# Kernel optimization log

Measured on AMD Instinct MI355X. Metric: run time of the kernel, lower is better.

## Reference

```python
import jax, jax.numpy as jnp
import numpy as np
from jax import lax

B, T, C = 32, 4096, 64
K, D, H, OUT = 256, 64, 512, 6

def _conv1d(x, w, b, stride):
    # x: [B, Cin, L], w: [Cout, Cin, k]
    y = lax.conv_general_dilated(x, w, (stride,), 'SAME',
                                 dimension_numbers=('NCH', 'OIH', 'NCH'))
    return y + b[None, :, None]

def _lstm_layer(x, wih, whh, b):
    # x: [B, T, in]; wih: [4H, in]; whh: [4H, H]
    Bb = x.shape[0]
    Hh = whh.shape[1]
    xg = jnp.einsum('bti,gi->btg', x, wih) + b          # [B, T, 4H] precomputed input gates
    def step(carry, g_t):
        h, c = carry
        gates = g_t + h @ whh.T
        i, f, g, o = jnp.split(gates, 4, axis=-1)        # torch gate order i,f,g,o
        i = jax.nn.sigmoid(i); f = jax.nn.sigmoid(f)
        g = jnp.tanh(g);       o = jax.nn.sigmoid(o)
        c = f * c + i * g
        h = o * jnp.tanh(c)
        return (h, c), h
    init = (jnp.zeros((Bb, Hh), x.dtype), jnp.zeros((Bb, Hh), x.dtype))
    _, hs = lax.scan(step, init, jnp.swapaxes(xg, 0, 1))
    return jnp.swapaxes(hs, 0, 1)                        # [B, T, H]

def setup_inputs() -> dict:
    key = jax.random.key(0)
    ks = jax.random.split(key, 12)
    s = 0.02
    return {
        'x':       jax.random.normal(ks[0], (B, T, C), jnp.float32),
        'conv_w1': jax.random.normal(ks[1], (64, 1, 4), jnp.float32) * s,
        'conv_b1': jnp.zeros((64,), jnp.float32),
        'conv_w2': jax.random.normal(ks[2], (64, 64, 4), jnp.float32) * s,
        'conv_b2': jnp.zeros((64,), jnp.float32),
        'conv_w3': jax.random.normal(ks[3], (64, 64, 3), jnp.float32) * s,
        'conv_b3': jnp.zeros((64,), jnp.float32),
        'codebook': jax.random.normal(ks[4], (K, D), jnp.float32),
        'wih0': jax.random.normal(ks[5], (4 * H, D), jnp.float32) * s,
        'whh0': jax.random.normal(ks[6], (4 * H, H), jnp.float32) * s,
        'bl0':  jnp.zeros((4 * H,), jnp.float32),
        'wih1': jax.random.normal(ks[7], (4 * H, H), jnp.float32) * s,
        'whh1': jax.random.normal(ks[8], (4 * H, H), jnp.float32) * s,
        'bl1':  jnp.zeros((4 * H,), jnp.float32),
        'w_out': jax.random.normal(ks[9], (OUT, H), jnp.float32) * s,
        'b_out': jnp.zeros((OUT,), jnp.float32),
    }

def reference(x, conv_w1, conv_b1, conv_w2, conv_b2, conv_w3, conv_b3,
              codebook, wih0, whh0, bl0, wih1, whh1, bl1, w_out, b_out):
    # ---- tokenizer (batched; replaces the per-sample python loop) ----
    sig = x.mean(axis=2)[:, None, :]                     # [B, 1, T] channel-mean 1D signal
    h1 = jax.nn.relu(_conv1d(sig, conv_w1, conv_b1, 2))   # [B, 64, T/2]
    h2 = jax.nn.relu(_conv1d(h1, conv_w2, conv_b2, 2))    # [B, 64, T/4]
    ze = _conv1d(h2, conv_w3, conv_b3, 1)                 # [B, D, T'] latents
    ze = jnp.swapaxes(ze, 1, 2)                           # [B, T', D]
    # nearest-code lookup: ||z - e||^2 argmin
    d = (jnp.sum(ze * ze, -1, keepdims=True)
         - 2.0 * ze @ codebook.T
         + jnp.sum(codebook * codebook, -1)[None, None, :])
    idx = jnp.argmin(d, axis=-1)                          # [B, T'] token indices
    # ---- codebook embedding gather ----
    z = codebook[idx]                                     # [B, T', D]
    # ---- 2-layer LSTM + per-step linear head ----
    h = _lstm_layer(z, wih0, whh0, bl0)
    h = _lstm_layer(h, wih1, whh1, bl1)
    preds = jnp.einsum('bth,oh->bto', h, w_out) + b_out   # [B, T', OUT]
    return preds
```

## Files before the change

kernel.cpp:

```cpp
#include <hip/hip_runtime.h>

constexpr int nB = 32, nT = 4096, nK = 256, nTP = 1024;

__device__ __forceinline__ float sigmoidf_(float x) { return 1.f / (1.f + expf(-x)); }

typedef unsigned int u32x4 __attribute__((ext_vector_type(4)));

__device__ __forceinline__ void store_u32_wt(unsigned* p, unsigned v) {
  asm volatile("global_store_dword %0, %1, off sc0 sc1" :: "v"(p), "v"(v) : "memory");
}
__device__ __forceinline__ void store_f32_wt(float* p, float v) {
  asm volatile("global_store_dword %0, %1, off sc0 sc1" :: "v"(p), "v"(v) : "memory");
}

__device__ __forceinline__ float dpp_xor1(float x) {
  return __int_as_float(__builtin_amdgcn_update_dpp(0, __float_as_int(x), 0xB1, 0xF, 0xF, true));
}
__device__ __forceinline__ float dpp_xor2(float x) {
  return __int_as_float(__builtin_amdgcn_update_dpp(0, __float_as_int(x), 0x4E, 0xF, 0xF, true));
}
__device__ __forceinline__ float dpp_xor8(float x) {
  return __int_as_float(__builtin_amdgcn_update_dpp(0, __float_as_int(x), 0x128, 0xF, 0xF, true));
}
__device__ __forceinline__ float swz_xor4(float x) {
  return __int_as_float(__builtin_amdgcn_ds_swizzle(__float_as_int(x), 0x101F));
}
__device__ __forceinline__ float swz_xor16(float x) {
  return __int_as_float(__builtin_amdgcn_ds_swizzle(__float_as_int(x), 0x401F));
}


__global__ __launch_bounds__(256) void k_mean(const float* __restrict__ x, float* __restrict__ sig) {
  int row = blockIdx.x * 4 + (threadIdx.x >> 6);
  int lane = threadIdx.x & 63;
  float v = x[(size_t)row * 64 + lane];
  #pragma unroll
  for (int off = 32; off > 0; off >>= 1) v += __shfl_down(v, off, 64);
  if (lane == 0) sig[row] = v * (1.0f / 64.0f);
}

__global__ __launch_bounds__(256) void k_conv1(const float* __restrict__ sig,
    const float* __restrict__ w1, const float* __restrict__ b1, float* __restrict__ h1) {
  int idx = blockIdx.x * 256 + threadIdx.x;
  int o = idx & 2047;
  int co = (idx >> 11) & 63;
  int b = idx >> 17;
  const float* s = sig + (size_t)b * nT;
  float acc = b1[co];
  int base = 2 * o - 1;
  #pragma unroll
  for (int j = 0; j < 4; j++) {
    int p = base + j;
    float sv = (p >= 0 && p < nT) ? s[p] : 0.f;
    acc = fmaf(w1[co * 4 + j], sv, acc);
  }
  h1[idx] = fmaxf(acc, 0.f);
}

__global__ __launch_bounds__(256) void k_conv2(const float* __restrict__ h1,
    const float* __restrict__ w2, const float* __restrict__ b2, float* __restrict__ h2) {
  int blk = blockIdx.x;
  int otile = blk & 3, co = (blk >> 2) & 63, b = blk >> 8;
  int o = otile * 256 + threadIdx.x;
  __shared__ float w[256];
  w[threadIdx.x] = w2[co * 256 + threadIdx.x];
  __syncthreads();
  const float* hin = h1 + (size_t)b * 64 * 2048;
  float acc = b2[co];
  int base = 2 * o - 1;
  for (int ci = 0; ci < 64; ci++) {
    const float* r = hin + ci * 2048;
    const float* wc = w + ci * 4;
    #pragma unroll
    for (int j = 0; j < 4; j++) {
      int p = base + j;
      float v = (p >= 0 && p < 2048) ? r[p] : 0.f;
      acc = fmaf(wc[j], v, acc);
    }
  }
  h2[((size_t)b * 64 + co) * 1024 + o] = fmaxf(acc, 0.f);
}

__global__ __launch_bounds__(256) void k_conv3(const float* __restrict__ h2,
    const float* __restrict__ w3, const float* __restrict__ b3, float* __restrict__ ze) {
  int blk = blockIdx.x;
  int otile = blk & 3, co = (blk >> 2) & 63, b = blk >> 8;
  int o = otile * 256 + threadIdx.x;
  __shared__ float w[192];
  if (threadIdx.x < 192) w[threadIdx.x] = w3[co * 192 + threadIdx.x];
  __syncthreads();
  const float* hin = h2 + (size_t)b * 64 * 1024;
  float acc = b3[co];
  for (int ci = 0; ci < 64; ci++) {
    const float* r = hin + ci * 1024;
    const float* wc = w + ci * 3;
    #pragma unroll
    for (int j = 0; j < 3; j++) {
      int p = o - 1 + j;
      float v = (p >= 0 && p < 1024) ? r[p] : 0.f;
      acc = fmaf(wc[j], v, acc);
    }
  }
  ze[((size_t)b * 64 + co) * 1024 + o] = acc;
}

__global__ __launch_bounds__(256) void k_cbnorm(const float* __restrict__ cb, float* __restrict__ cbn) {
  int k = threadIdx.x;
  const float4* c4 = (const float4*)(cb + (size_t)k * 64);
  float acc = 0.f;
  #pragma unroll
  for (int q = 0; q < 16; q++) {
    float4 e = c4[q];
    acc = fmaf(e.x, e.x, fmaf(e.y, e.y, fmaf(e.z, e.z, fmaf(e.w, e.w, acc))));
  }
  cbn[k] = acc;
}

__global__ __launch_bounds__(256) void k_vq(const float* __restrict__ ze,
    const float* __restrict__ cb, const float* __restrict__ cbn, float* __restrict__ zq) {
  __shared__ float scb[nK * 64];
  for (int i = threadIdx.x; i < nK * 64; i += 256) scb[i] = cb[i];
  __syncthreads();
  int g = blockIdx.x * 256 + threadIdx.x;
  int b = g >> 10, o = g & 1023;
  const float* zb = ze + (size_t)b * 64 * 1024 + o;
  float z[64];
  #pragma unroll
  for (int d = 0; d < 64; d++) z[d] = zb[(size_t)d * 1024];
  float best = 3.4e38f; int bi = 0;
  for (int k = 0; k < nK; k++) {
    const float4* ck = (const float4*)(scb + k * 64);
    float dot = 0.f;
    #pragma unroll
    for (int q = 0; q < 16; q++) {
      float4 c4 = ck[q];
      dot = fmaf(c4.x, z[4 * q + 0], dot);
      dot = fmaf(c4.y, z[4 * q + 1], dot);
      dot = fmaf(c4.z, z[4 * q + 2], dot);
      dot = fmaf(c4.w, z[4 * q + 3], dot);
    }
    float s = cbn[k] - 2.f * dot;
    if (s < best) { best = s; bi = k; }
  }
  float4* zo4 = (float4*)(zq + (size_t)g * 64);
  const float4* cbest = (const float4*)(scb + bi * 64);
  #pragma unroll
  for (int q = 0; q < 16; q++) zo4[q] = cbest[q];
}

__global__ __launch_bounds__(256) void k_zqt(const float* __restrict__ zq, float* __restrict__ zqT) {
  int t = blockIdx.x;
  for (int o = threadIdx.x; o < 2048; o += 256) {
    int d = o >> 5, b = o & 31;
    zqT[(size_t)t * 2048 + o] = zq[((size_t)b * nTP + t) * 64 + d];
  }
}


__global__ __launch_bounds__(512, 2) void k_lstm(
    const float* __restrict__ zqT,
    const float* __restrict__ wih0, const float* __restrict__ whh0, const float* __restrict__ bl0,
    const float* __restrict__ wih1, const float* __restrict__ whh1, const float* __restrict__ bl1,
    const float* __restrict__ wout, const float* __restrict__ bout,
    float* __restrict__ st, float* __restrict__ out)
{
  __shared__ float wB [2][4][32][36];
  __shared__ float wAh[2][4][32][20];
  __shared__ float wAz[2][4][64];
  __shared__ float wHd[2][512];
  __shared__ float bHd[2];
  __shared__ float h0s[16384];

  float* h0T = st;
  float* h1T = st + 32768;
  unsigned* flags = (unsigned*)(st + 65536);

  const int blk = blockIdx.x;
  const int tid = threadIdx.x;
  const int dim = tid >> 8;
  const int bg  = (tid >> 5) & 7;
  const int c   = tid & 31;
  const int b0  = bg * 4;
  const int j   = 2 * blk + dim;

  for (int idx = tid; idx < 2 * 4 * 32 * 32; idx += 512) {
    int k = idx & 31, cc = (idx >> 5) & 31, gg = (idx >> 10) & 3, dd = idx >> 12;
    int row = gg * 512 + 2 * blk + dd;
    float v = (cc < 16) ? whh1[(size_t)row * 512 + cc * 32 + k]
                        : wih1[(size_t)row * 512 + (cc - 16) * 32 + k];
    wB[dd][gg][cc][k] = v;
  }
  for (int idx = tid; idx < 2 * 4 * 32 * 16; idx += 512) {
    int k = idx & 15, cc = (idx >> 4) & 31, gg = (idx >> 9) & 3, dd = idx >> 11;
    wAh[dd][gg][cc][k] = whh0[(size_t)(gg * 512 + 2 * blk + dd) * 512 + cc * 16 + k];
  }
  if (tid < 512) {
    int d = tid & 63, gg = (tid >> 6) & 3, dd = tid >> 8;
    wAz[dd][gg][d] = wih0[(size_t)(gg * 512 + 2 * blk + dd) * 64 + d];
  }
  if (blk < 96) {
    for (int idx = tid; idx < 1024; idx += 512) {
      int q = idx >> 9, i = idx & 511;
      int p = blk * 2 + q;
      wHd[q][i] = wout[(size_t)(p >> 5) * 512 + i];
      if (i == 0) bHd[q] = bout[p >> 5];
    }
  }
  float bA[4], bB4[4];
  #pragma unroll
  for (int g = 0; g < 4; g++) { bA[g] = bl0[g * 512 + j]; bB4[g] = bl1[g * 512 + j]; }
  float creg0 = 0.f, creg1 = 0.f;
  __syncthreads();

  const float* h0vL0 = h0s + ((c * 512 + b0) ^ ((c & 7) << 2));
  const int cp = c - 16;
  const float* h0vA = h0s + (((cp < 0 ? 0 : cp) * 1024 + b0) ^ (((2 * (cp < 0 ? 0 : cp)) & 7) << 2));
  const float* h0vB = h0s + (((cp < 0 ? 0 : cp) * 1024 + 512 + b0) ^ (((2 * (cp < 0 ? 0 : cp) + 1) & 7) << 2));

  for (int t = 0; t <= nTP + 1; t++) {
    if (t <= nTP) {
      const float* src = h0T + (t & 1) * 16384;
      #pragma unroll
      for (int q = 0; q < 8; q++) {
        int lin = (q * 512 + tid) * 4;
        float4 v = *(const float4*)(src + lin);
        int phys = lin ^ (((lin >> 9) & 7) << 2);
        *(float4*)&h0s[phys] = v;
      }
      __syncthreads();
    }

    if (t < nTP) {
      float acc[16];
      #pragma unroll
      for (int r = 0; r < 16; r++) acc[r] = 0.f;
      {
        #pragma unroll
        for (int s = 0; s < 4; s++) {
          float4 v0 = *(const float4*)(h0vL0 + (s * 4 + 0) * 32);
          float4 v1 = *(const float4*)(h0vL0 + (s * 4 + 1) * 32);
          float4 v2 = *(const float4*)(h0vL0 + (s * 4 + 2) * 32);
          float4 v3 = *(const float4*)(h0vL0 + (s * 4 + 3) * 32);
          #pragma unroll
          for (int g = 0; g < 4; g++) {
            float4 w = *(const float4*)&wAh[dim][g][c][s * 4];
            float* a = acc + g * 4;
            a[0]=fmaf(w.x,v0.x,a[0]); a[0]=fmaf(w.y,v1.x,a[0]); a[0]=fmaf(w.z,v2.x,a[0]); a[0]=fmaf(w.w,v3.x,a[0]);
            a[1]=fmaf(w.x,v0.y,a[1]); a[1]=fmaf(w.y,v1.y,a[1]); a[1]=fmaf(w.z,v2.y,a[1]); a[1]=fmaf(w.w,v3.y,a[1]);
            a[2]=fmaf(w.x,v0.z,a[2]); a[2]=fmaf(w.y,v1.z,a[2]); a[2]=fmaf(w.z,v2.z,a[2]); a[2]=fmaf(w.w,v3.z,a[2]);
            a[3]=fmaf(w.x,v0.w,a[3]); a[3]=fmaf(w.y,v1.w,a[3]); a[3]=fmaf(w.z,v2.w,a[3]); a[3]=fmaf(w.w,v3.w,a[3]);
          }
        }
      }
      {
        const float* zt = zqT + (size_t)t * 2048 + b0;
        float4 u0 = *(const float4*)(zt + (c * 2 + 0) * 32);
        float4 u1 = *(const float4*)(zt + (c * 2 + 1) * 32);
        #pragma unroll
        for (int g = 0; g < 4; g++) {
          float wx = wAz[dim][g][c * 2 + 0], wy = wAz[dim][g][c * 2 + 1];
          float* a = acc + g * 4;
          a[0]=fmaf(wx,u0.x,a[0]); a[0]=fmaf(wy,u1.x,a[0]);
          a[1]=fmaf(wx,u0.y,a[1]); a[1]=fmaf(wy,u1.y,a[1]);
          a[2]=fmaf(wx,u0.z,a[2]); a[2]=fmaf(wy,u1.z,a[2]);
          a[3]=fmaf(wx,u0.w,a[3]); a[3]=fmaf(wy,u1.w,a[3]);
        }
      }
      #pragma unroll
      for (int r = 0; r < 16; r++) acc[r] += dpp_xor1(acc[r]);
      #pragma unroll
      for (int r = 0; r < 16; r++) acc[r] += dpp_xor2(acc[r]);
      #pragma unroll
      for (int r = 0; r < 16; r++) acc[r] += swz_xor4(acc[r]);
      #pragma unroll
      for (int r = 0; r < 16; r++) acc[r] += dpp_xor8(acc[r]);
      #pragma unroll
      for (int r = 0; r < 16; r++) acc[r] += swz_xor16(acc[r]);
      if (c < 4) {
        int b = b0 + c;
        float gi = sigmoidf_(acc[0 * 4 + c] + bA[0]);
        float gf = sigmoidf_(acc[1 * 4 + c] + bA[1]);
        float gg = tanhf    (acc[2 * 4 + c] + bA[2]);
        float go = sigmoidf_(acc[3 * 4 + c] + bA[3]);
        float cn = fmaf(gf, creg0, gi * gg);
        creg0 = cn;
        store_f32_wt(h0T + ((t + 1) & 1) * 16384 + j * 32 + b, go * tanhf(cn));
      }
    }

    if (t >= 1 && t <= nTP) {
      const float* h1p = h1T + ((t - 1) & 1) * 16384;
      float4 vbuf[32];
      if (c < 16) {
        const float* vg = h1p + c * 32 * 32 + b0;
        #pragma unroll
        for (int k = 0; k < 32; k++) vbuf[k] = *(const float4*)(vg + k * 32);
      } else {
        #pragma unroll
        for (int k = 0; k < 16; k++) vbuf[k] = *(const float4*)(h0vA + k * 32);
        #pragma unroll
        for (int k = 0; k < 16; k++) vbuf[16 + k] = *(const float4*)(h0vB + k * 32);
      }
      float acc[16];
      #pragma unroll
      for (int r = 0; r < 16; r++) acc[r] = 0.f;
      #pragma unroll
      for (int s = 0; s < 8; s++) {
        float4 v0 = vbuf[s * 4 + 0];
        float4 v1 = vbuf[s * 4 + 1];
        float4 v2 = vbuf[s * 4 + 2];
        float4 v3 = vbuf[s * 4 + 3];
        #pragma unroll
        for (int g = 0; g < 4; g++) {
          float4 w = *(const float4*)&wB[dim][g][c][s * 4];
          float* a = acc + g * 4;
          a[0]=fmaf(w.x,v0.x,a[0]); a[0]=fmaf(w.y,v1.x,a[0]); a[0]=fmaf(w.z,v2.x,a[0]); a[0]=fmaf(w.w,v3.x,a[0]);
          a[1]=fmaf(w.x,v0.y,a[1]); a[1]=fmaf(w.y,v1.y,a[1]); a[1]=fmaf(w.z,v2.y,a[1]); a[1]=fmaf(w.w,v3.y,a[1]);
          a[2]=fmaf(w.x,v0.z,a[2]); a[2]=fmaf(w.y,v1.z,a[2]); a[2]=fmaf(w.z,v2.z,a[2]); a[2]=fmaf(w.w,v3.z,a[2]);
          a[3]=fmaf(w.x,v0.w,a[3]); a[3]=fmaf(w.y,v1.w,a[3]); a[3]=fmaf(w.z,v2.w,a[3]); a[3]=fmaf(w.w,v3.w,a[3]);
        }
      }
      #pragma unroll
      for (int r = 0; r < 16; r++) acc[r] += dpp_xor1(acc[r]);
      #pragma unroll
      for (int r = 0; r < 16; r++) acc[r] += dpp_xor2(acc[r]);
      #pragma unroll
      for (int r = 0; r < 16; r++) acc[r] += swz_xor4(acc[r]);
      #pragma unroll
      for (int r = 0; r < 16; r++) acc[r] += dpp_xor8(acc[r]);
      #pragma unroll
      for (int r = 0; r < 16; r++) acc[r] += swz_xor16(acc[r]);
      if (c < 4) {
        int b = b0 + c;
        float gi = sigmoidf_(acc[0 * 4 + c] + bB4[0]);
        float gf = sigmoidf_(acc[1 * 4 + c] + bB4[1]);
        float gg = tanhf    (acc[2 * 4 + c] + bB4[2]);
        float go = sigmoidf_(acc[3 * 4 + c] + bB4[3]);
        float cn = fmaf(gf, creg1, gi * gg);
        creg1 = cn;
        store_f32_wt(h1T + (t & 1) * 16384 + j * 32 + b, go * tanhf(cn));
      }
    }

    asm volatile("s_waitcnt vmcnt(0)" ::: "memory");
    __syncthreads();

    if (t <= nTP && tid == 0) store_u32_wt(flags + blk, (unsigned)(t + 1));

    if (t >= 2 && blk < 96 && tid >= 64 && tid < 80) {
      int q = (tid >> 3) & 1, l = tid & 7;
      int p = blk * 2 + q;
      int b = p & 31;
      const float* h1s = h1T + ((t - 1) & 1) * 16384;
      float a = 0.f;
      #pragma unroll 8
      for (int m = 0; m < 64; m++) {
        int i = l * 64 + m;
        a = fmaf(wHd[q][i], h1s[i * 32 + b], a);
      }
      a += __shfl_down(a, 4, 8);
      a += __shfl_down(a, 2, 8);
      a += __shfl_down(a, 1, 8);
      if (l == 0) out[((size_t)b * nTP + (t - 2)) * 6 + (p >> 5)] = a + bHd[q];
    }

    if (t <= nTP) {
      unsigned tgt = (unsigned)(t + 1);
      if (tid < 64) {
        const u32x4* fp = (const u32x4*)flags + tid;
        for (;;) {
          u32x4 f;
          asm volatile("global_load_dwordx4 %0, %1, off sc0 sc1\n\ts_waitcnt vmcnt(0)"
                       : "=&v"(f) : "v"(fp) : "memory");
          bool ok = (f.x >= tgt) && (f.y >= tgt) && (f.z >= tgt) && (f.w >= tgt);
          if (__all(ok)) break;
          __builtin_amdgcn_s_sleep(1);
        }
        __builtin_amdgcn_fence(__ATOMIC_ACQUIRE, "agent");
      }
      __syncthreads();
    }
  }
}


extern "C" void kernel_launch(void* const* d_in, const int* in_sizes, int n_in,
                              void* d_out, int out_size, void* d_ws, size_t ws_size,
                              hipStream_t stream) {
  (void)in_sizes; (void)n_in; (void)out_size; (void)ws_size;
  const float* x    = (const float*)d_in[0];
  const float* w1   = (const float*)d_in[1];
  const float* b1   = (const float*)d_in[2];
  const float* w2   = (const float*)d_in[3];
  const float* b2   = (const float*)d_in[4];
  const float* w3   = (const float*)d_in[5];
  const float* b3   = (const float*)d_in[6];
  const float* cb   = (const float*)d_in[7];
  const float* wih0 = (const float*)d_in[8];
  const float* whh0 = (const float*)d_in[9];
  const float* bl0  = (const float*)d_in[10];
  const float* wih1 = (const float*)d_in[11];
  const float* whh1 = (const float*)d_in[12];
  const float* bl1  = (const float*)d_in[13];
  const float* wout = (const float*)d_in[14];
  const float* bout = (const float*)d_in[15];
  float* out = (float*)d_out;

  float* ws  = (float*)d_ws;
  float* sig = ws;
  float* h1c = sig + 131072;
  float* h2c = h1c + 4194304;
  float* ze  = h2c + 2097152;
  float* zq  = ze  + 2097152;
  float* cbn = zq  + 2097152;
  float* stp = ws;
  float* zqT = h1c;

  k_mean <<<32768, 256, 0, stream>>>(x, sig);
  k_conv1<<<16384, 256, 0, stream>>>(sig, w1, b1, h1c);
  hipMemsetAsync(stp, 0, (65536 + 1024) * sizeof(float), stream);
  k_conv2<<<8192, 256, 0, stream>>>(h1c, w2, b2, h2c);
  k_conv3<<<8192, 256, 0, stream>>>(h2c, w3, b3, ze);
  k_cbnorm<<<1, 256, 0, stream>>>(cb, cbn);
  k_vq   <<<128, 256, 0, stream>>>(ze, cb, cbn, zq);
  k_zqt  <<<1024, 256, 0, stream>>>(zq, zqT);

  void* kargs[] = { (void*)&zqT, (void*)&wih0, (void*)&whh0, (void*)&bl0,
                    (void*)&wih1, (void*)&whh1, (void*)&bl1,
                    (void*)&wout, (void*)&bout, (void*)&stp, (void*)&out };
  hipLaunchCooperativeKernel((void*)k_lstm, dim3(256), dim3(512), kargs, 0, stream);
}
```

Before: 16.54 ms.

## Split LSTM block into per-layer wavefront teams and prefetch global loads early

Instead of every wave computing both the layer-0 and layer-1 recurrences in sequence, the block is split into two teams: team 0 does layer 0 for 8 batches per wave, and team 1 does layer 1 for both hidden units. The two layers' work can then run concurrently on different waves within each timestep. The global loads of h1 and zq are issued before the h0 staging barrier to hide their latency. Doubling the accumulators to 32 per thread raises register pressure, so launch bounds drop to one block per SM, which cuts occupancy.

```diff
diff --git a/kernel.cpp b/kernel.cpp
--- a/kernel.cpp
+++ b/kernel.cpp
@@ -157,7 +157,7 @@
 }
 
 
-__global__ __launch_bounds__(512, 2) void k_lstm(
+__global__ __launch_bounds__(512, 1) void k_lstm(
     const float* __restrict__ zqT,
     const float* __restrict__ wih0, const float* __restrict__ whh0, const float* __restrict__ bl0,
     const float* __restrict__ wih1, const float* __restrict__ whh1, const float* __restrict__ bl1,
@@ -175,13 +175,15 @@
   float* h1T = st + 32768;
   unsigned* flags = (unsigned*)(st + 65536);
 
-  const int blk = blockIdx.x;
-  const int tid = threadIdx.x;
-  const int dim = tid >> 8;
-  const int bg  = (tid >> 5) & 7;
-  const int c   = tid & 31;
-  const int b0  = bg * 4;
-  const int j   = 2 * blk + dim;
+  const int blk  = blockIdx.x;
+  const int tid  = threadIdx.x;
+  const int team = tid >> 8;
+  const int grp  = (tid >> 5) & 7;
+  const int c    = tid & 31;
+  const int dimA = grp & 1;
+  const int b0A  = (grp >> 1) * 8;
+  const int b0B  = grp * 4;
+  const int jA   = 2 * blk + dimA;
 
   for (int idx = tid; idx < 2 * 4 * 32 * 32; idx += 512) {
     int k = idx & 31, cc = (idx >> 5) & 31, gg = (idx >> 10) & 3, dd = idx >> 12;
@@ -206,18 +208,39 @@
       if (i == 0) bHd[q] = bout[p >> 5];
     }
   }
-  float bA[4], bB4[4];
-  #pragma unroll
-  for (int g = 0; g < 4; g++) { bA[g] = bl0[g * 512 + j]; bB4[g] = bl1[g * 512 + j]; }
-  float creg0 = 0.f, creg1 = 0.f;
+  float bA[4], bB4d[2][4];
+  #pragma unroll
+  for (int g = 0; g < 4; g++) {
+    bA[g] = bl0[g * 512 + jA];
+    #pragma unroll
+    for (int dd = 0; dd < 2; dd++) bB4d[dd][g] = bl1[g * 512 + 2 * blk + dd];
+  }
+  float creg0 = 0.f;
+  float creg1[2] = {0.f, 0.f};
   __syncthreads();
 
-  const float* h0vL0 = h0s + ((c * 512 + b0) ^ ((c & 7) << 2));
-  const int cp = c - 16;
-  const float* h0vA = h0s + (((cp < 0 ? 0 : cp) * 1024 + b0) ^ (((2 * (cp < 0 ? 0 : cp)) & 7) << 2));
-  const float* h0vB = h0s + (((cp < 0 ? 0 : cp) * 1024 + 512 + b0) ^ (((2 * (cp < 0 ? 0 : cp) + 1) & 7) << 2));
+  const float* p0a = h0s + ((c * 512 + b0A) ^ ((c & 7) << 2));
+  const float* p0b = h0s + ((c * 512 + b0A + 4) ^ ((c & 7) << 2));
+  const int cp = (c < 16) ? 0 : (c - 16);
+  const float* pA = h0s + ((cp * 1024 + b0B) ^ (((2 * cp) & 7) << 2));
+  const float* pB = h0s + ((cp * 1024 + 512 + b0B) ^ (((2 * cp + 1) & 7) << 2));
 
   for (int t = 0; t <= nTP + 1; t++) {
+    float4 vbuf[32];
+    if (team == 1 && t >= 1 && t <= nTP && c < 16) {
+      const float* vg = h1T + ((t - 1) & 1) * 16384 + c * 32 * 32 + b0B;
+      #pragma unroll
+      for (int k = 0; k < 32; k++) vbuf[k] = *(const float4*)(vg + k * 32);
+    }
+    float4 u0a, u0b, u1a, u1b;
+    if (team == 0 && t < nTP) {
+      const float* zt = zqT + (size_t)t * 2048 + b0A;
+      u0a = *(const float4*)(zt + (c * 2 + 0) * 32);
+      u0b = *(const float4*)(zt + (c * 2 + 0) * 32 + 4);
+      u1a = *(const float4*)(zt + (c * 2 + 1) * 32);
+      u1b = *(const float4*)(zt + (c * 2 + 1) * 32 + 4);
+    }
+
     if (t <= nTP) {
       const float* src = h0T + (t & 1) * 16384;
       #pragma unroll
@@ -230,21 +253,93 @@
       __syncthreads();
     }
 
-    if (t < nTP) {
-      float acc[16];
-      #pragma unroll
-      for (int r = 0; r < 16; r++) acc[r] = 0.f;
+    if (team == 0 && t < nTP) {
+      float acc[32];
+      #pragma unroll
+      for (int r = 0; r < 32; r++) acc[r] = 0.f;
+      #pragma unroll
+      for (int s = 0; s < 4; s++) {
+        float4 v0a = *(const float4*)(p0a + (s * 4 + 0) * 32);
+        float4 v0b = *(const float4*)(p0b + (s * 4 + 0) * 32);
+        float4 v1a = *(const float4*)(p0a + (s * 4 + 1) * 32);
+        float4 v1b = *(const float4*)(p0b + (s * 4 + 1) * 32);
+        float4 v2a = *(const float4*)(p0a + (s * 4 + 2) * 32);
+        float4 v2b = *(const float4*)(p0b + (s * 4 + 2) * 32);
+        float4 v3a = *(const float4*)(p0a + (s * 4 + 3) * 32);
+        float4 v3b = *(const float4*)(p0b + (s * 4 + 3) * 32);
+        #pragma unroll
+        for (int g = 0; g < 4; g++) {
+          float4 w = *(const float4*)&wAh[dimA][g][c][s * 4];
+          float* a = acc + g * 8;
+          a[0]=fmaf(w.x,v0a.x,a[0]); a[0]=fmaf(w.y,v1a.x,a[0]); a[0]=fmaf(w.z,v2a.x,a[0]); a[0]=fmaf(w.w,v3a.x,a[0]);
+          a[1]=fmaf(w.x,v0a.y,a[1]); a[1]=fmaf(w.y,v1a.y,a[1]); a[1]=fmaf(w.z,v2a.y,a[1]); a[1]=fmaf(w.w,v3a.y,a[1]);
+          a[2]=fmaf(w.x,v0a.z,a[2]); a[2]=fmaf(w.y,v1a.z,a[2]); a[2]=fmaf(w.z,v2a.z,a[2]); a[2]=fmaf(w.w,v3a.z,a[2]);
+          a[3]=fmaf(w.x,v0a.w,a[3]); a[3]=fmaf(w.y,v1a.w,a[3]); a[3]=fmaf(w.z,v2a.w,a[3]); a[3]=fmaf(w.w,v3a.w,a[3]);
+          a[4]=fmaf(w.x,v0b.x,a[4]); a[4]=fmaf(w.y,v1b.x,a[4]); a[4]=fmaf(w.z,v2b.x,a[4]); a[4]=fmaf(w.w,v3b.x,a[4]);
+          a[5]=fmaf(w.x,v0b.y,a[5]); a[5]=fmaf(w.y,v1b.y,a[5]); a[5]=fmaf(w.z,v2b.y,a[5]); a[5]=fmaf(w.w,v3b.y,a[5]);
+          a[6]=fmaf(w.x,v0b.z,a[6]); a[6]=fmaf(w.y,v1b.z,a[6]); a[6]=fmaf(w.z,v2b.z,a[6]); a[6]=fmaf(w.w,v3b.z,a[6]);
+          a[7]=fmaf(w.x,v0b.w,a[7]); a[7]=fmaf(w.y,v1b.w,a[7]); a[7]=fmaf(w.z,v2b.w,a[7]); a[7]=fmaf(w.w,v3b.w,a[7]);
+        }
+      }
       {
         #pragma unroll
-        for (int s = 0; s < 4; s++) {
-          float4 v0 = *(const float4*)(h0vL0 + (s * 4 + 0) * 32);
-          float4 v1 = *(const float4*)(h0vL0 + (s * 4 + 1) * 32);
-          float4 v2 = *(const float4*)(h0vL0 + (s * 4 + 2) * 32);
-          float4 v3 = *(const float4*)(h0vL0 + (s * 4 + 3) * 32);
+        for (int g = 0; g < 4; g++) {
+          float wx = wAz[dimA][g][c * 2 + 0], wy = wAz[dimA][g][c * 2 + 1];
+          float* a = acc + g * 8;
+          a[0]=fmaf(wx,u0a.x,a[0]); a[0]=fmaf(wy,u1a.x,a[0]);
+          a[1]=fmaf(wx,u0a.y,a[1]); a[1]=fmaf(wy,u1a.y,a[1]);
+          a[2]=fmaf(wx,u0a.z,a[2]); a[2]=fmaf(wy,u1a.z,a[2]);
+          a[3]=fmaf(wx,u0a.w,a[3]); a[3]=fmaf(wy,u1a.w,a[3]);
+          a[4]=fmaf(wx,u0b.x,a[4]); a[4]=fmaf(wy,u1b.x,a[4]);
+          a[5]=fmaf(wx,u0b.y,a[5]); a[5]=fmaf(wy,u1b.y,a[5]);
+          a[6]=fmaf(wx,u0b.z,a[6]); a[6]=fmaf(wy,u1b.z,a[6]);
+          a[7]=fmaf(wx,u0b.w,a[7]); a[7]=fmaf(wy,u1b.w,a[7]);
+        }
+      }
+      #pragma unroll
+      for (int r = 0; r < 32; r++) acc[r] += dpp_xor1(acc[r]);
+      #pragma unroll
+      for (int r = 0; r < 32; r++) acc[r] += dpp_xor2(acc[r]);
+      #pragma unroll
+      for (int r = 0; r < 32; r++) acc[r] += swz_xor4(acc[r]);
+      #pragma unroll
+      for (int r = 0; r < 32; r++) acc[r] += dpp_xor8(acc[r]);
+      #pragma unroll
+      for (int r = 0; r < 32; r++) acc[r] += swz_xor16(acc[r]);
+      if (c < 8) {
+        int b = b0A + c;
+        float gi = sigmoidf_(acc[0 * 8 + c] + bA[0]);
+        float gf = sigmoidf_(acc[1 * 8 + c] + bA[1]);
+        float gg = tanhf    (acc[2 * 8 + c] + bA[2]);
+        float go = sigmoidf_(acc[3 * 8 + c] + bA[3]);
+        float cn = fmaf(gf, creg0, gi * gg);
+        creg0 = cn;
+        store_f32_wt(h0T + ((t + 1) & 1) * 16384 + jA * 32 + b, go * tanhf(cn));
+      }
+    }
+
+    if (team == 1 && t >= 1 && t <= nTP) {
+      if (c >= 16) {
+        #pragma unroll
+        for (int k = 0; k < 16; k++) vbuf[k] = *(const float4*)(pA + k * 32);
+        #pragma unroll
+        for (int k = 0; k < 16; k++) vbuf[16 + k] = *(const float4*)(pB + k * 32);
+      }
+      float acc[32];
+      #pragma unroll
+      for (int r = 0; r < 32; r++) acc[r] = 0.f;
+      #pragma unroll
+      for (int s = 0; s < 8; s++) {
+        float4 v0 = vbuf[s * 4 + 0];
+        float4 v1 = vbuf[s * 4 + 1];
+        float4 v2 = vbuf[s * 4 + 2];
+        float4 v3 = vbuf[s * 4 + 3];
+        #pragma unroll
+        for (int dd = 0; dd < 2; dd++) {
           #pragma unroll
           for (int g = 0; g < 4; g++) {
-            float4 w = *(const float4*)&wAh[dim][g][c][s * 4];
-            float* a = acc + g * 4;
+            float4 w = *(const float4*)&wB[dd][g][c][s * 4];
+            float* a = acc + dd * 16 + g * 4;
             a[0]=fmaf(w.x,v0.x,a[0]); a[0]=fmaf(w.y,v1.x,a[0]); a[0]=fmaf(w.z,v2.x,a[0]); a[0]=fmaf(w.w,v3.x,a[0]);
             a[1]=fmaf(w.x,v0.y,a[1]); a[1]=fmaf(w.y,v1.y,a[1]); a[1]=fmaf(w.z,v2.y,a[1]); a[1]=fmaf(w.w,v3.y,a[1]);
             a[2]=fmaf(w.x,v0.z,a[2]); a[2]=fmaf(w.y,v1.z,a[2]); a[2]=fmaf(w.z,v2.z,a[2]); a[2]=fmaf(w.w,v3.z,a[2]);
@@ -252,93 +347,28 @@
           }
         }
       }
-      {
-        const float* zt = zqT + (size_t)t * 2048 + b0;
-        float4 u0 = *(const float4*)(zt + (c * 2 + 0) * 32);
-        float4 u1 = *(const float4*)(zt + (c * 2 + 1) * 32);
-        #pragma unroll
-        for (int g = 0; g < 4; g++) {
-          float wx = wAz[dim][g][c * 2 + 0], wy = wAz[dim][g][c * 2 + 1];
-          float* a = acc + g * 4;
-          a[0]=fmaf(wx,u0.x,a[0]); a[0]=fmaf(wy,u1.x,a[0]);
-          a[1]=fmaf(wx,u0.y,a[1]); a[1]=fmaf(wy,u1.y,a[1]);
-          a[2]=fmaf(wx,u0.z,a[2]); a[2]=fmaf(wy,u1.z,a[2]);
-          a[3]=fmaf(wx,u0.w,a[3]); a[3]=fmaf(wy,u1.w,a[3]);
+      #pragma unroll
+      for (int r = 0; r < 32; r++) acc[r] += dpp_xor1(acc[r]);
+      #pragma unroll
+      for (int r = 0; r < 32; r++) acc[r] += dpp_xor2(acc[r]);
+      #pragma unroll
+      for (int r = 0; r < 32; r++) acc[r] += swz_xor4(acc[r]);
+      #pragma unroll
+      for (int r = 0; r < 32; r++) acc[r] += dpp_xor8(acc[r]);
+      #pragma unroll
+      for (int r = 0; r < 32; r++) acc[r] += swz_xor16(acc[r]);
+      if (c < 4) {
+        int b = b0B + c;
+        #pragma unroll
+        for (int dd = 0; dd < 2; dd++) {
+          float gi = sigmoidf_(acc[dd * 16 + 0 * 4 + c] + bB4d[dd][0]);
+          float gf = sigmoidf_(acc[dd * 16 + 1 * 4 + c] + bB4d[dd][1]);
+          float gg = tanhf    (acc[dd * 16 + 2 * 4 + c] + bB4d[dd][2]);
+          float go = sigmoidf_(acc[dd * 16 + 3 * 4 + c] + bB4d[dd][3]);
+          float cn = fmaf(gf, creg1[dd], gi * gg);
+          creg1[dd] = cn;
+          store_f32_wt(h1T + (t & 1) * 16384 + (2 * blk + dd) * 32 + b, go * tanhf(cn));
         }
-      }
-      #pragma unroll
-      for (int r = 0; r < 16; r++) acc[r] += dpp_xor1(acc[r]);
-      #pragma unroll
-      for (int r = 0; r < 16; r++) acc[r] += dpp_xor2(acc[r]);
-      #pragma unroll
-      for (int r = 0; r < 16; r++) acc[r] += swz_xor4(acc[r]);
-      #pragma unroll
-      for (int r = 0; r < 16; r++) acc[r] += dpp_xor8(acc[r]);
-      #pragma unroll
-      for (int r = 0; r < 16; r++) acc[r] += swz_xor16(acc[r]);
-      if (c < 4) {
-        int b = b0 + c;
-        float gi = sigmoidf_(acc[0 * 4 + c] + bA[0]);
-        float gf = sigmoidf_(acc[1 * 4 + c] + bA[1]);
-        float gg = tanhf    (acc[2 * 4 + c] + bA[2]);
-        float go = sigmoidf_(acc[3 * 4 + c] + bA[3]);
-        float cn = fmaf(gf, creg0, gi * gg);
-        creg0 = cn;
-        store_f32_wt(h0T + ((t + 1) & 1) * 16384 + j * 32 + b, go * tanhf(cn));
-      }
-    }
-
-    if (t >= 1 && t <= nTP) {
-      const float* h1p = h1T + ((t - 1) & 1) * 16384;
-      float4 vbuf[32];
-      if (c < 16) {
-        const float* vg = h1p + c * 32 * 32 + b0;
-        #pragma unroll
-        for (int k = 0; k < 32; k++) vbuf[k] = *(const float4*)(vg + k * 32);
-      } else {
-        #pragma unroll
-        for (int k = 0; k < 16; k++) vbuf[k] = *(const float4*)(h0vA + k * 32);
-        #pragma unroll
-        for (int k = 0; k < 16; k++) vbuf[16 + k] = *(const float4*)(h0vB + k * 32);
-      }
-      float acc[16];
-      #pragma unroll
-      for (int r = 0; r < 16; r++) acc[r] = 0.f;
-      #pragma unroll
-      for (int s = 0; s < 8; s++) {
-        float4 v0 = vbuf[s * 4 + 0];
-        float4 v1 = vbuf[s * 4 + 1];
-        float4 v2 = vbuf[s * 4 + 2];
-        float4 v3 = vbuf[s * 4 + 3];
-        #pragma unroll
-        for (int g = 0; g < 4; g++) {
-          float4 w = *(const float4*)&wB[dim][g][c][s * 4];
-          float* a = acc + g * 4;
-          a[0]=fmaf(w.x,v0.x,a[0]); a[0]=fmaf(w.y,v1.x,a[0]); a[0]=fmaf(w.z,v2.x,a[0]); a[0]=fmaf(w.w,v3.x,a[0]);
-          a[1]=fmaf(w.x,v0.y,a[1]); a[1]=fmaf(w.y,v1.y,a[1]); a[1]=fmaf(w.z,v2.y,a[1]); a[1]=fmaf(w.w,v3.y,a[1]);
-          a[2]=fmaf(w.x,v0.z,a[2]); a[2]=fmaf(w.y,v1.z,a[2]); a[2]=fmaf(w.z,v2.z,a[2]); a[2]=fmaf(w.w,v3.z,a[2]);
-          a[3]=fmaf(w.x,v0.w,a[3]); a[3]=fmaf(w.y,v1.w,a[3]); a[3]=fmaf(w.z,v2.w,a[3]); a[3]=fmaf(w.w,v3.w,a[3]);
-        }
-      }
-      #pragma unroll
-      for (int r = 0; r < 16; r++) acc[r] += dpp_xor1(acc[r]);
-      #pragma unroll
-      for (int r = 0; r < 16; r++) acc[r] += dpp_xor2(acc[r]);
-      #pragma unroll
-      for (int r = 0; r < 16; r++) acc[r] += swz_xor4(acc[r]);
-      #pragma unroll
-      for (int r = 0; r < 16; r++) acc[r] += dpp_xor8(acc[r]);
-      #pragma unroll
-      for (int r = 0; r < 16; r++) acc[r] += swz_xor16(acc[r]);
-      if (c < 4) {
-        int b = b0 + c;
-        float gi = sigmoidf_(acc[0 * 4 + c] + bB4[0]);
-        float gf = sigmoidf_(acc[1 * 4 + c] + bB4[1]);
-        float gg = tanhf    (acc[2 * 4 + c] + bB4[2]);
-        float go = sigmoidf_(acc[3 * 4 + c] + bB4[3]);
-        float cn = fmaf(gf, creg1, gi * gg);
-        creg1 = cn;
-        store_f32_wt(h1T + (t & 1) * 16384 + j * 32 + b, go * tanhf(cn));
       }
     }
 
```

Result: slower. 25.86 ms (+56.3%).
